# Performance work log

Measured on AMD Instinct MI355X. Metric: run time of the kernel, lower is better.

The kernel has to match this reference:

```python
import jax, jax.numpy as jnp
import numpy as np

E = 512      # embed dim
H = 8        # heads
DH = E // H  # dim per head
LN_EPS = 1e-5


def _sinusoidal_pe(pos_seq, embed_dim):
    # pos_seq: (L,) float; returns (L, embed_dim)
    inv_freq = 1.0 / (10000.0 ** (jnp.arange(0.0, embed_dim, 2.0, dtype=jnp.float32) / embed_dim))
    sin_inp = jnp.outer(pos_seq, inv_freq)                     # (L, Dh/2)
    return jnp.concatenate([jnp.sin(sin_inp), jnp.cos(sin_inp)], axis=-1)


def _rel_shift_bhij(x, k_len):
    # x: (B, H, T, L) -> left-shift trick -> (B, H, T, k_len)
    b, h, t, l = x.shape
    x = jnp.pad(x, ((0, 0), (0, 0), (0, 0), (1, 0)))           # (B,H,T,L+1)
    x = x.reshape(b, h, l + 1, t)
    x = x[:, :, 1:, :]
    x = x.reshape(b, h, t, l)
    return x[:, :, :, :k_len]


def setup_inputs() -> dict:
    key = jax.random.key(0)
    ks = jax.random.split(key, 10)
    B, T = 8, 1024
    xav = np.sqrt(6.0 / (E + E))  # xavier_uniform bound for (E,E)
    return {
        "input_tensor": jax.random.normal(ks[0], (B, T, E), jnp.float32),
        "sequence_mask": jnp.ones((B, T), dtype=bool),
        "ln_scale": jnp.ones((E,), jnp.float32),
        "ln_bias": jnp.zeros((E,), jnp.float32),
        "q_w": jax.random.uniform(ks[1], (E, E), jnp.float32, -xav, xav),
        "k_w": jax.random.uniform(ks[2], (E, E), jnp.float32, -xav, xav),
        "v_w": jax.random.uniform(ks[3], (E, E), jnp.float32, -xav, xav),
        "in_proj_bias": jax.random.normal(ks[4], (3 * E,), jnp.float32) * 0.02,
        "out_w": jax.random.uniform(ks[5], (E, E), jnp.float32, -xav, xav),
        "out_b": jnp.zeros((E,), jnp.float32),
        "pos_bias_u": jax.random.normal(ks[6], (H, DH), jnp.float32) * 0.02,
        "pos_bias_v": jax.random.normal(ks[7], (H, DH), jnp.float32) * 0.02,
    }


def reference(input_tensor, sequence_mask, ln_scale, ln_bias, q_w, k_w, v_w,
              in_proj_bias, out_w, out_b, pos_bias_u, pos_bias_v):
    B, T, _ = input_tensor.shape
    # LayerNorm
    mu = jnp.mean(input_tensor, axis=-1, keepdims=True)
    var = jnp.mean(jnp.square(input_tensor - mu), axis=-1, keepdims=True)
    x = (input_tensor - mu) * jax.lax.rsqrt(var + LN_EPS) * ln_scale + ln_bias

    # note: torch code unpacks in_proj_bias as (bias_k, bias_q, bias_v)
    bias_k, bias_q, bias_v = jnp.split(in_proj_bias, 3)
    q = (x @ q_w.T + bias_q).reshape(B, T, H, DH)
    k = (x @ k_w.T + bias_k).reshape(B, T, H, DH)
    v = (x @ v_w.T + bias_v).reshape(B, T, H, DH)

    # sinusoidal relative PE: positions T-1 .. -(T-1), shape (2T-1, Dh)
    pos_seq = jnp.arange(T - 1, -T, -1, dtype=jnp.float32)
    rel_pe = _sinusoidal_pe(pos_seq, DH)

    q_u = q + pos_bias_u  # (B,T,H,Dh)
    q_v = q + pos_bias_v

    attn_ac = jnp.einsum('bihf,bjhf->bhij', q_u, k)            # (B,H,T,T)
    attn_bd = jnp.einsum('bihf,jf->bhij', q_v, rel_pe)         # (B,H,T,2T-1)
    attn_bd = _rel_shift_bhij(attn_bd, k_len=T)                # (B,H,T,T)

    mask = jnp.where(sequence_mask[:, None, None, :], 0.0, -jnp.inf).astype(input_tensor.dtype)
    attn = (attn_ac + attn_bd + mask) * (1.0 / np.sqrt(DH))
    weights = jax.nn.softmax(attn, axis=-1)

    out = jnp.einsum('bhij,bjhf->bihf', weights, v).reshape(B, T, E)
    return out @ out_w.T + out_b
```

## Files before the change

kernel.cpp:

```cpp
#include <hip/hip_runtime.h>
#include <hip/hip_bf16.h>
#include <cstdint>
#include <cstddef>


typedef __attribute__((ext_vector_type(8))) short bf16x8;
typedef __attribute__((ext_vector_type(4))) float f32x4;
typedef __attribute__((ext_vector_type(4))) unsigned short usht4;

#define MFMA(a, b, c) __builtin_amdgcn_mfma_f32_16x16x32_bf16((a), (b), (c), 0, 0, 0)

__device__ __forceinline__ unsigned short f2bf(float f) {
    __bf16 h = (__bf16)f;
    union { __bf16 h; unsigned short u; } v; v.h = h;
    return v.u;
}

__device__ __forceinline__ float exp2r(float x) {
    float r; asm("v_exp_f32 %0, %1" : "=v"(r) : "v"(x)); return r;
}

__device__ __forceinline__ void gload16(void* lds, const void* g) {
    __builtin_amdgcn_global_load_lds((const __attribute__((address_space(1))) void*)g,
                                     (__attribute__((address_space(3))) void*)lds,
                                     16, 0, 0);
}

__global__ __launch_bounds__(256) void prep_ln_kernel(const float* __restrict__ qw,
                                                      const float* __restrict__ kw,
                                                      const float* __restrict__ vw,
                                                      const float* __restrict__ ow,
                                                      const float* __restrict__ x,
                                                      const float* __restrict__ gam,
                                                      const float* __restrict__ bet,
                                                      unsigned short* __restrict__ wcat,
                                                      unsigned short* __restrict__ kptab,
                                                      float* __restrict__ qsc,
                                                      unsigned short* __restrict__ xout) {
    const int bid = blockIdx.x;
    if (bid < 4096) {
        const int which = bid >> 10;
        const int idx = (bid & 1023) * 256 + threadIdx.x;
        const float* src = (which == 0) ? qw : (which == 1) ? kw : (which == 2) ? vw : ow;
        wcat[which * 262144 + idx] = f2bf(src[idx]);
        return;
    }
    if (bid < 4352) {
        const int idx = (bid - 4096) * 256 + threadIdx.x;
        const int t = idx >> 6, f6 = idx & 63, f = f6 & 31;
        const float w = powf(10000.0f, -(float)f * (1.0f / 32.0f));
        const float ang = (float)t * w;
        const float sv = sinf(ang), cv = cosf(ang);
        qsc[t * 64 + 2 * f + ((f6 < 32) ? 0 : 1)] = (f6 < 32) ? sv : cv;
        kptab[idx] = f2bf((f6 < 32) ? cv : sv);
        return;
    }
    const int row = (bid - 4352) * 4 + (threadIdx.x >> 6);
    const int lane = threadIdx.x & 63;
    const float4* xr = (const float4*)(x + (size_t)row * 512);
    float4 a = xr[lane];
    float4 b = xr[lane + 64];
    float s  = a.x + a.y + a.z + a.w + b.x + b.y + b.z + b.w;
    float ss = a.x*a.x + a.y*a.y + a.z*a.z + a.w*a.w
             + b.x*b.x + b.y*b.y + b.z*b.z + b.w*b.w;
#pragma unroll
    for (int m = 1; m < 64; m <<= 1) {
        s  += __shfl_xor(s, m);
        ss += __shfl_xor(ss, m);
    }
    const float mu   = s * (1.0f / 512.0f);
    const float rstd = rsqrtf(ss * (1.0f / 512.0f) - mu * mu + 1e-5f);
    const float4* g4 = (const float4*)gam;
    const float4* b4 = (const float4*)bet;
    float4 g0 = g4[lane], g1 = g4[lane + 64];
    float4 c0 = b4[lane], c1 = b4[lane + 64];
    usht4 o0, o1;
    o0[0] = f2bf((a.x - mu) * rstd * g0.x + c0.x);
    o0[1] = f2bf((a.y - mu) * rstd * g0.y + c0.y);
    o0[2] = f2bf((a.z - mu) * rstd * g0.z + c0.z);
    o0[3] = f2bf((a.w - mu) * rstd * g0.w + c0.w);
    o1[0] = f2bf((b.x - mu) * rstd * g1.x + c1.x);
    o1[1] = f2bf((b.y - mu) * rstd * g1.y + c1.y);
    o1[2] = f2bf((b.z - mu) * rstd * g1.z + c1.z);
    o1[3] = f2bf((b.w - mu) * rstd * g1.w + c1.w);
    *(usht4*)&xout[(size_t)row * 512 + lane * 4] = o0;
    *(usht4*)&xout[(size_t)row * 512 + 256 + lane * 4] = o1;
}

#define GEMM_PROLOGUE()                                                        \
    __shared__ __align__(16) unsigned short As[2][128 * 64];                   \
    __shared__ __align__(16) unsigned short Bs[2][128 * 64];                   \
    const int tid = threadIdx.x;                                               \
    const int wid = tid >> 6;                                                  \
    const int lane = tid & 63;                                                 \
    const int wr = wid >> 1, wc = wid & 1;                                     \
    const int c = lane & 15, hi = lane >> 4;                                   \
    f32x4 acc[4][4];                                                           \
    _Pragma("unroll") for (int i = 0; i < 4; ++i)                              \
        _Pragma("unroll") for (int j = 0; j < 4; ++j) acc[i][j] = 0.0f;        \
    const int rbase = wid * 8;                                                 \
    const int sl = lane & 7;                                                   \
    const int lrow = lane >> 3;                                                \
    auto stageAB = [&](int buf, int kt) {                                      \
        const int k0 = kt * 64;                                                \
        _Pragma("unroll") for (int ch = 0; ch < 4; ++ch) {                     \
            const int rr = ch * 32 + rbase + lrow;                             \
            const int soff = (sl * 8) ^ ((rr & 7) << 3);                       \
            gload16(&As[buf][(ch * 32 + rbase) * 64],                          \
                    A + (size_t)(m0 + rr) * 512 + k0 + soff);                  \
            gload16(&Bs[buf][(ch * 32 + rbase) * 64],                          \
                    Bw + (size_t)(n0 + rr) * 512 + k0 + soff);                 \
        }                                                                      \
    };                                                                         \
    stageAB(0, 0);                                                             \
    __syncthreads();                                                           \
    int cb = 0;                                                                \
    for (int kt = 0; kt < 8; ++kt) {                                           \
        if (kt < 7) stageAB(cb ^ 1, kt + 1);                                   \
        _Pragma("unroll") for (int ks = 0; ks < 2; ++ks) {                     \
            bf16x8 af[4], bfr[4];                                              \
            _Pragma("unroll") for (int mf = 0; mf < 4; ++mf) {                 \
                const int ar = wr * 64 + mf * 16 + c;                          \
                const int ko = (ks * 32 + hi * 8) ^ ((ar & 7) << 3);           \
                af[mf] = *(const bf16x8*)&As[cb][ar * 64 + ko];                \
            }                                                                  \
            _Pragma("unroll") for (int nf = 0; nf < 4; ++nf) {                 \
                const int br = wc * 64 + nf * 16 + c;                          \
                const int ko = (ks * 32 + hi * 8) ^ ((br & 7) << 3);           \
                bfr[nf] = *(const bf16x8*)&Bs[cb][br * 64 + ko];               \
            }                                                                  \
            _Pragma("unroll") for (int mf = 0; mf < 4; ++mf)                   \
                _Pragma("unroll") for (int nf = 0; nf < 4; ++nf)               \
                    acc[mf][nf] = MFMA(af[mf], bfr[nf], acc[mf][nf]);          \
        }                                                                      \
        __syncthreads();                                                       \
        cb ^= 1;                                                               \
    }                                                                          \
    const int mb = m0 + wr * 64;                                               \
    const int nb = n0 + wc * 64;

__global__ __launch_bounds__(256) void gemm_qkv_kernel(const unsigned short* __restrict__ A,
                                                       const unsigned short* __restrict__ Bw,
                                                       const float* __restrict__ ipb,
                                                       const float* __restrict__ pbu,
                                                       const float* __restrict__ pbv,
                                                       const float* __restrict__ qsc,
                                                       unsigned short* __restrict__ qu,
                                                       unsigned short* __restrict__ qp,
                                                       unsigned short* __restrict__ kk,
                                                       unsigned short* __restrict__ vT) {
    const int m0 = blockIdx.x * 128;
    const int n0 = blockIdx.y * 128;
    const int nsec = blockIdx.y >> 2;
    GEMM_PROLOGUE()

    const float SCALE = 0.125f * 1.44269504088896340736f;

    if (nsec == 0) {
#pragma unroll
        for (int mf = 0; mf < 4; ++mf) {
#pragma unroll
            for (int r = 0; r < 4; ++r) {
                const int gm = mb + mf * 16 + hi * 4 + r;
                const int t = gm & 1023;
#pragma unroll
                for (int p = 0; p < 2; ++p) {
                    const int fl = p * 16 + c;
                    const int gn1 = nb + fl;
                    const int gn2 = gn1 + 32;
                    const float v1 = acc[mf][p][r]     + ipb[512 + gn1];
                    const float v2 = acc[mf][p + 2][r] + ipb[512 + gn2];
                    qu[(size_t)gm * 512 + gn1] = f2bf((v1 + pbu[gn1]) * SCALE);
                    qu[(size_t)gm * 512 + gn2] = f2bf((v2 + pbu[gn2]) * SCALE);
                    const float qvs = v1 + pbv[gn1];
                    const float qvc = v2 + pbv[gn2];
                    const float2 sc2 = *(const float2*)&qsc[t * 64 + 2 * fl];
                    qp[(size_t)gm * 512 + gn1] = f2bf((qvs * sc2.x + qvc * sc2.y) * SCALE);
                    qp[(size_t)gm * 512 + gn2] = f2bf((qvc * sc2.x - qvs * sc2.y) * SCALE);
                }
            }
        }
    } else if (nsec == 1) {
#pragma unroll
        for (int mf = 0; mf < 4; ++mf)
#pragma unroll
            for (int nf = 0; nf < 4; ++nf) {
                const int gm = mb + mf * 16 + hi * 4;
                const int gn = nb + nf * 16 + c;
                const float bia = ipb[gn - 512];
#pragma unroll
                for (int r = 0; r < 4; ++r)
                    kk[(size_t)(gm + r) * 512 + (gn - 512)] = f2bf(acc[mf][nf][r] + bia);
            }
    } else {
#pragma unroll
        for (int mf = 0; mf < 4; ++mf)
#pragma unroll
            for (int nf = 0; nf < 4; ++nf) {
                const int gm = mb + mf * 16 + hi * 4;
                const int gn = nb + nf * 16 + c;
                const float bia = ipb[gn];
                const int bb = gm >> 10;
                const int t  = gm & 1023;
                usht4 pk;
#pragma unroll
                for (int r = 0; r < 4; ++r) pk[r] = f2bf(acc[mf][nf][r] + bia);
                *(usht4*)&vT[((size_t)bb * 512 + (gn - 1024)) * 1024 + t] = pk;
            }
    }
}

__global__ __launch_bounds__(256) void gemm_out_kernel(const unsigned short* __restrict__ A,
                                                       const unsigned short* __restrict__ Bw,
                                                       const float* __restrict__ bias,
                                                       float* __restrict__ outf) {
    const int m0 = blockIdx.x * 128;
    const int n0 = blockIdx.y * 128;
    GEMM_PROLOGUE()
#pragma unroll
    for (int mf = 0; mf < 4; ++mf)
#pragma unroll
        for (int nf = 0; nf < 4; ++nf) {
            const int gm = mb + mf * 16 + hi * 4;
            const int gn = nb + nf * 16 + c;
            const float bia = bias[gn];
#pragma unroll
            for (int r = 0; r < 4; ++r)
                outf[(size_t)(gm + r) * 512 + gn] = acc[mf][nf][r] + bia;
        }
}

__global__ __launch_bounds__(512, 4) void attn_kernel(const unsigned short* __restrict__ qu,
                                                      const unsigned short* __restrict__ qp,
                                                      const unsigned short* __restrict__ kk,
                                                      const unsigned short* __restrict__ vT,
                                                      const unsigned short* __restrict__ kptab,
                                                      unsigned short* __restrict__ att) {
    __shared__ __align__(16) char smem[67584];
    char* kbuf = smem;
    char* pbuf = smem + 16384;
    char* vbuf = smem + 32768;
    unsigned short* pw = (unsigned short*)(smem + 49152) + (threadIdx.x >> 6) * (16 * 72);

    const int tid = threadIdx.x;
    const int w = tid >> 6, lane = tid & 63;
    const int c = lane & 15, hi = lane >> 4;
    const int id = blockIdx.x;
    const int b = id & 7, h = (id >> 3) & 7, it = id >> 6;
    const int iw = it * 128 + w * 16;

    const size_t qbase = ((size_t)b * 1024 + iw) * 512 + h * 64;
    bf16x8 quf[4];
#pragma unroll
    for (int ks = 0; ks < 2; ++ks) {
        const size_t o = qbase + (size_t)c * 512 + ks * 32 + hi * 8;
        quf[ks]     = *(const bf16x8*)&qu[o];
        quf[ks + 2] = *(const bf16x8*)&qp[o];
    }

    f32x4 oacc[4];
    float mrun[4], lrun[4];
#pragma unroll
    for (int nf = 0; nf < 4; ++nf) oacc[nf] = 0.0f;
#pragma unroll
    for (int r = 0; r < 4; ++r) { mrun[r] = -1e30f; lrun[r] = 0.0f; }

    bf16x8 ones;
#pragma unroll
    for (int i = 0; i < 8; ++i) ones[i] = (short)0x3F80;

    int off2[2][4];
#pragma unroll
    for (int nf = 0; nf < 4; ++nf) {
        const int r = nf * 16 + c;
        const int sw = (r & 7) << 4;
        off2[0][nf] = r * 128 + ((hi * 16) ^ sw);
        off2[1][nf] = r * 128 + ((64 + hi * 16) ^ sw);
    }

    const size_t kbase = ((size_t)b * 1024) * 512 + h * 64;
    const size_t vbase = ((size_t)b * 512 + h * 64) * 1024;

    const int srow = tid >> 3;
    const int scol = ((tid & 7) * 16) ^ ((srow & 7) << 4);
    const char* ksrc = (const char*)(kk + kbase + (size_t)srow * 512) + scol;
    const char* psrc = (const char*)(kptab + (size_t)srow * 64) + scol;
    const char* vsrc = (const char*)(vT + vbase + (size_t)srow * 1024) + scol;

    auto stage = [&](int buf, int jt) {
        gload16(kbuf + buf * 8192 + w * 1024, ksrc + (size_t)jt * 65536);
        gload16(pbuf + buf * 8192 + w * 1024, psrc + (size_t)jt * 8192);
        gload16(vbuf + buf * 8192 + w * 1024, vsrc + (size_t)jt * 128);
    };

    stage(0, 0);
    __syncthreads();
    int cur = 0;

    for (int jt = 0; jt < 16; ++jt) {
        if (jt < 15) stage(cur ^ 1, jt + 1);

        const char* kb = kbuf + cur * 8192;
        const char* pb = pbuf + cur * 8192;
        const char* vb = vbuf + cur * 8192;

        f32x4 s[4];
#pragma unroll
        for (int nf = 0; nf < 4; ++nf) s[nf] = 0.0f;
#pragma unroll
        for (int ks = 0; ks < 4; ++ks) {
            const char* base = (ks < 2) ? kb : pb;
            bf16x8 kfr[4];
#pragma unroll
            for (int nf = 0; nf < 4; ++nf)
                kfr[nf] = *(const bf16x8*)(base + off2[ks & 1][nf]);
#pragma unroll
            for (int nf = 0; nf < 4; ++nf)
                s[nf] = MFMA(quf[ks], kfr[nf], s[nf]);
        }

        float lm[4];
        bool allok = true;
#pragma unroll
        for (int r = 0; r < 4; ++r) {
            lm[r] = fmaxf(fmaxf(s[0][r], s[1][r]), fmaxf(s[2][r], s[3][r]));
            allok = allok && (lm[r] <= mrun[r] + 8.0f);
        }
        if (!__all(allok)) {
#pragma unroll
            for (int r = 0; r < 4; ++r) {
                float pm = lm[r];
                pm = fmaxf(pm, __shfl_xor(pm, 1));
                pm = fmaxf(pm, __shfl_xor(pm, 2));
                pm = fmaxf(pm, __shfl_xor(pm, 4));
                pm = fmaxf(pm, __shfl_xor(pm, 8));
                const float mn = fmaxf(mrun[r], pm);
                const float sc = exp2r(mrun[r] - mn);
                mrun[r] = mn;
                lrun[r] *= sc;
#pragma unroll
                for (int nf = 0; nf < 4; ++nf) oacc[nf][r] *= sc;
            }
        }

#pragma unroll
        for (int nf = 0; nf < 4; ++nf)
#pragma unroll
            for (int r = 0; r < 4; ++r)
                pw[(hi * 4 + r) * 72 + nf * 16 + c] = f2bf(exp2r(s[nf][r] - mrun[r]));

        f32x4 psum = 0.0f;
#pragma unroll
        for (int ks = 0; ks < 2; ++ks) {
            const bf16x8 pa = *(const bf16x8*)&pw[c * 72 + ks * 32 + hi * 8];
            bf16x8 vfr[4];
#pragma unroll
            for (int nf = 0; nf < 4; ++nf)
                vfr[nf] = *(const bf16x8*)(vb + off2[ks][nf]);
#pragma unroll
            for (int nf = 0; nf < 4; ++nf)
                oacc[nf] = MFMA(pa, vfr[nf], oacc[nf]);
            psum = MFMA(pa, ones, psum);
        }
#pragma unroll
        for (int r = 0; r < 4; ++r) lrun[r] += psum[r];

        __syncthreads();
        cur ^= 1;
    }

#pragma unroll
    for (int r = 0; r < 4; ++r) {
        const float inv = 1.0f / lrun[r];
#pragma unroll
        for (int nf = 0; nf < 4; ++nf)
            att[((size_t)b * 1024 + iw + hi * 4 + r) * 512 + h * 64 + nf * 16 + c] =
                f2bf(oacc[nf][r] * inv);
    }
}

extern "C" void kernel_launch(void* const* d_in, const int* in_sizes, int n_in,
                              void* d_out, int out_size, void* d_ws, size_t ws_size,
                              hipStream_t stream) {
    const float* x_in = (const float*)d_in[0];
    const float* ln_g = (const float*)d_in[2];
    const float* ln_b = (const float*)d_in[3];
    const float* q_w  = (const float*)d_in[4];
    const float* k_w  = (const float*)d_in[5];
    const float* v_w  = (const float*)d_in[6];
    const float* ipb  = (const float*)d_in[7];
    const float* o_w  = (const float*)d_in[8];
    const float* o_b  = (const float*)d_in[9];
    const float* pbu  = (const float*)d_in[10];
    const float* pbv  = (const float*)d_in[11];
    float* out = (float*)d_out;

    char* ws = (char*)d_ws;
    unsigned short* xb    = (unsigned short*)(ws);
    unsigned short* qu    = (unsigned short*)(ws + 8388608);
    unsigned short* qp    = (unsigned short*)(ws + 16777216);
    unsigned short* kk    = (unsigned short*)(ws + 25165824);
    unsigned short* vT    = (unsigned short*)(ws + 33554432);
    unsigned short* wcat  = (unsigned short*)(ws + 41943040);
    unsigned short* kptab = (unsigned short*)(ws + 44040192);
    float*          qsc   = (float*)(ws + 44171264);
    unsigned short* att   = xb;

    prep_ln_kernel<<<dim3(6400), 256, 0, stream>>>(q_w, k_w, v_w, o_w, x_in, ln_g, ln_b,
                                                   wcat, kptab, qsc, xb);
    gemm_qkv_kernel<<<dim3(64, 12), 256, 0, stream>>>(xb, wcat, ipb, pbu, pbv, qsc,
                                                      qu, qp, kk, vT);
    attn_kernel<<<dim3(512), 512, 0, stream>>>(qu, qp, kk, vT, kptab, att);
    gemm_out_kernel<<<dim3(64, 4), 256, 0, stream>>>(att, wcat + 786432, o_b, out);
}
```

Baseline: 86.03 us.

## Give each attention wave two 16-row query tiles, halving block threads

The attention kernel now launches 256-thread blocks in which each wave processes 32 query rows as two 16-row MFMA tiles instead of one. Each K/positional/V fragment read from LDS is reused across both tiles, and each thread issues two staging loads per buffer so the block still fills the same 128-row tile. This cuts LDS fragment reads per MFMA and the number of waves synchronising at each barrier. In exchange it doubles the accumulator and softmax-state registers per thread, which may lower occupancy and latency hiding.

```diff
diff --git a/kernel.cpp b/kernel.cpp
--- a/kernel.cpp
+++ b/kernel.cpp
@@ -230,7 +230,7 @@
         }
 }
 
-__global__ __launch_bounds__(512, 4) void attn_kernel(const unsigned short* __restrict__ qu,
+__global__ __launch_bounds__(256, 2) void attn_kernel(const unsigned short* __restrict__ qu,
                                                       const unsigned short* __restrict__ qp,
                                                       const unsigned short* __restrict__ kk,
                                                       const unsigned short* __restrict__ vT,
@@ -240,30 +240,35 @@
     char* kbuf = smem;
     char* pbuf = smem + 16384;
     char* vbuf = smem + 32768;
-    unsigned short* pw = (unsigned short*)(smem + 49152) + (threadIdx.x >> 6) * (16 * 72);
+    unsigned short* pw = (unsigned short*)(smem + 49152) + (threadIdx.x >> 6) * (32 * 72);
 
     const int tid = threadIdx.x;
     const int w = tid >> 6, lane = tid & 63;
     const int c = lane & 15, hi = lane >> 4;
     const int id = blockIdx.x;
     const int b = id & 7, h = (id >> 3) & 7, it = id >> 6;
-    const int iw = it * 128 + w * 16;
+    const int iw = it * 128 + w * 32;
 
     const size_t qbase = ((size_t)b * 1024 + iw) * 512 + h * 64;
-    bf16x8 quf[4];
-#pragma unroll
-    for (int ks = 0; ks < 2; ++ks) {
-        const size_t o = qbase + (size_t)c * 512 + ks * 32 + hi * 8;
-        quf[ks]     = *(const bf16x8*)&qu[o];
-        quf[ks + 2] = *(const bf16x8*)&qp[o];
-    }
-
-    f32x4 oacc[4];
-    float mrun[4], lrun[4];
-#pragma unroll
-    for (int nf = 0; nf < 4; ++nf) oacc[nf] = 0.0f;
-#pragma unroll
-    for (int r = 0; r < 4; ++r) { mrun[r] = -1e30f; lrun[r] = 0.0f; }
+    bf16x8 quf[2][4];
+#pragma unroll
+    for (int mi = 0; mi < 2; ++mi)
+#pragma unroll
+        for (int ks = 0; ks < 2; ++ks) {
+            const size_t o = qbase + (size_t)(mi * 16 + c) * 512 + ks * 32 + hi * 8;
+            quf[mi][ks]     = *(const bf16x8*)&qu[o];
+            quf[mi][ks + 2] = *(const bf16x8*)&qp[o];
+        }
+
+    f32x4 oacc[2][4];
+    float mrun[2][4], lrun[2][4];
+#pragma unroll
+    for (int mi = 0; mi < 2; ++mi) {
+#pragma unroll
+        for (int nf = 0; nf < 4; ++nf) oacc[mi][nf] = 0.0f;
+#pragma unroll
+        for (int r = 0; r < 4; ++r) { mrun[mi][r] = -1e30f; lrun[mi][r] = 0.0f; }
+    }
 
     bf16x8 ones;
 #pragma unroll
@@ -283,14 +288,23 @@
 
     const int srow = tid >> 3;
     const int scol = ((tid & 7) * 16) ^ ((srow & 7) << 4);
-    const char* ksrc = (const char*)(kk + kbase + (size_t)srow * 512) + scol;
-    const char* psrc = (const char*)(kptab + (size_t)srow * 64) + scol;
-    const char* vsrc = (const char*)(vT + vbase + (size_t)srow * 1024) + scol;
+    const char* ksrc  = (const char*)(kk + kbase + (size_t)srow * 512) + scol;
+    const char* ksrc2 = ksrc + 32 * 1024;
+    const char* psrc  = (const char*)(kptab + (size_t)srow * 64) + scol;
+    const char* psrc2 = psrc + 32 * 128;
+    const char* vsrc  = (const char*)(vT + vbase + (size_t)srow * 1024) + scol;
+    const char* vsrc2 = vsrc + 32 * 2048;
 
     auto stage = [&](int buf, int jt) {
-        gload16(kbuf + buf * 8192 + w * 1024, ksrc + (size_t)jt * 65536);
-        gload16(pbuf + buf * 8192 + w * 1024, psrc + (size_t)jt * 8192);
-        gload16(vbuf + buf * 8192 + w * 1024, vsrc + (size_t)jt * 128);
+        const size_t ko = (size_t)jt * 65536;
+        const size_t po = (size_t)jt * 8192;
+        const size_t vo = (size_t)jt * 128;
+        gload16(kbuf + buf * 8192 + w * 1024,        ksrc  + ko);
+        gload16(kbuf + buf * 8192 + 4096 + w * 1024, ksrc2 + ko);
+        gload16(pbuf + buf * 8192 + w * 1024,        psrc  + po);
+        gload16(pbuf + buf * 8192 + 4096 + w * 1024, psrc2 + po);
+        gload16(vbuf + buf * 8192 + w * 1024,        vsrc  + vo);
+        gload16(vbuf + buf * 8192 + 4096 + w * 1024, vsrc2 + vo);
     };
 
     stage(0, 0);
@@ -304,9 +318,11 @@
         const char* pb = pbuf + cur * 8192;
         const char* vb = vbuf + cur * 8192;
 
-        f32x4 s[4];
-#pragma unroll
-        for (int nf = 0; nf < 4; ++nf) s[nf] = 0.0f;
+        f32x4 s[2][4];
+#pragma unroll
+        for (int mi = 0; mi < 2; ++mi)
+#pragma unroll
+            for (int nf = 0; nf < 4; ++nf) s[mi][nf] = 0.0f;
 #pragma unroll
         for (int ks = 0; ks < 4; ++ks) {
             const char* base = (ks < 2) ? kb : pb;
@@ -315,68 +331,88 @@
             for (int nf = 0; nf < 4; ++nf)
                 kfr[nf] = *(const bf16x8*)(base + off2[ks & 1][nf]);
 #pragma unroll
+            for (int mi = 0; mi < 2; ++mi)
+#pragma unroll
+                for (int nf = 0; nf < 4; ++nf)
+                    s[mi][nf] = MFMA(quf[mi][ks], kfr[nf], s[mi][nf]);
+        }
+
+        bool allok = true;
+        float lm[2][4];
+#pragma unroll
+        for (int mi = 0; mi < 2; ++mi)
+#pragma unroll
+            for (int r = 0; r < 4; ++r) {
+                lm[mi][r] = fmaxf(fmaxf(s[mi][0][r], s[mi][1][r]),
+                                  fmaxf(s[mi][2][r], s[mi][3][r]));
+                allok = allok && (lm[mi][r] <= mrun[mi][r] + 8.0f);
+            }
+        if (!__all(allok)) {
+#pragma unroll
+            for (int mi = 0; mi < 2; ++mi)
+#pragma unroll
+                for (int r = 0; r < 4; ++r) {
+                    float pm = lm[mi][r];
+                    pm = fmaxf(pm, __shfl_xor(pm, 1));
+                    pm = fmaxf(pm, __shfl_xor(pm, 2));
+                    pm = fmaxf(pm, __shfl_xor(pm, 4));
+                    pm = fmaxf(pm, __shfl_xor(pm, 8));
+                    const float mn = fmaxf(mrun[mi][r], pm);
+                    const float sc = exp2r(mrun[mi][r] - mn);
+                    mrun[mi][r] = mn;
+                    lrun[mi][r] *= sc;
+#pragma unroll
+                    for (int nf = 0; nf < 4; ++nf) oacc[mi][nf][r] *= sc;
+                }
+        }
+
+#pragma unroll
+        for (int mi = 0; mi < 2; ++mi)
+#pragma unroll
             for (int nf = 0; nf < 4; ++nf)
-                s[nf] = MFMA(quf[ks], kfr[nf], s[nf]);
-        }
-
-        float lm[4];
-        bool allok = true;
-#pragma unroll
-        for (int r = 0; r < 4; ++r) {
-            lm[r] = fmaxf(fmaxf(s[0][r], s[1][r]), fmaxf(s[2][r], s[3][r]));
-            allok = allok && (lm[r] <= mrun[r] + 8.0f);
-        }
-        if (!__all(allok)) {
-#pragma unroll
-            for (int r = 0; r < 4; ++r) {
-                float pm = lm[r];
-                pm = fmaxf(pm, __shfl_xor(pm, 1));
-                pm = fmaxf(pm, __shfl_xor(pm, 2));
-                pm = fmaxf(pm, __shfl_xor(pm, 4));
-                pm = fmaxf(pm, __shfl_xor(pm, 8));
-                const float mn = fmaxf(mrun[r], pm);
-                const float sc = exp2r(mrun[r] - mn);
-                mrun[r] = mn;
-                lrun[r] *= sc;
-#pragma unroll
-                for (int nf = 0; nf < 4; ++nf) oacc[nf][r] *= sc;
-            }
-        }
-
-#pragma unroll
-        for (int nf = 0; nf < 4; ++nf)
-#pragma unroll
-            for (int r = 0; r < 4; ++r)
-                pw[(hi * 4 + r) * 72 + nf * 16 + c] = f2bf(exp2r(s[nf][r] - mrun[r]));
-
-        f32x4 psum = 0.0f;
+#pragma unroll
+                for (int r = 0; r < 4; ++r)
+                    pw[(mi * 16 + hi * 4 + r) * 72 + nf * 16 + c] =
+                        f2bf(exp2r(s[mi][nf][r] - mrun[mi][r]));
+
+        f32x4 psum[2] = {0.0f, 0.0f};
 #pragma unroll
         for (int ks = 0; ks < 2; ++ks) {
-            const bf16x8 pa = *(const bf16x8*)&pw[c * 72 + ks * 32 + hi * 8];
+            bf16x8 pa[2];
+#pragma unroll
+            for (int mi = 0; mi < 2; ++mi)
+                pa[mi] = *(const bf16x8*)&pw[(mi * 16 + c) * 72 + ks * 32 + hi * 8];
             bf16x8 vfr[4];
 #pragma unroll
             for (int nf = 0; nf < 4; ++nf)
                 vfr[nf] = *(const bf16x8*)(vb + off2[ks][nf]);
 #pragma unroll
-            for (int nf = 0; nf < 4; ++nf)
-                oacc[nf] = MFMA(pa, vfr[nf], oacc[nf]);
-            psum = MFMA(pa, ones, psum);
-        }
-#pragma unroll
-        for (int r = 0; r < 4; ++r) lrun[r] += psum[r];
+            for (int mi = 0; mi < 2; ++mi) {
+#pragma unroll
+                for (int nf = 0; nf < 4; ++nf)
+                    oacc[mi][nf] = MFMA(pa[mi], vfr[nf], oacc[mi][nf]);
+                psum[mi] = MFMA(pa[mi], ones, psum[mi]);
+            }
+        }
+#pragma unroll
+        for (int mi = 0; mi < 2; ++mi)
+#pragma unroll
+            for (int r = 0; r < 4; ++r) lrun[mi][r] += psum[mi][r];
 
         __syncthreads();
         cur ^= 1;
     }
 
 #pragma unroll
-    for (int r = 0; r < 4; ++r) {
-        const float inv = 1.0f / lrun[r];
-#pragma unroll
-        for (int nf = 0; nf < 4; ++nf)
-            att[((size_t)b * 1024 + iw + hi * 4 + r) * 512 + h * 64 + nf * 16 + c] =
-                f2bf(oacc[nf][r] * inv);
-    }
+    for (int mi = 0; mi < 2; ++mi)
+#pragma unroll
+        for (int r = 0; r < 4; ++r) {
+            const float inv = 1.0f / lrun[mi][r];
+#pragma unroll
+            for (int nf = 0; nf < 4; ++nf)
+                att[((size_t)b * 1024 + iw + mi * 16 + hi * 4 + r) * 512 + h * 64 + nf * 16 + c] =
+                    f2bf(oacc[mi][nf][r] * inv);
+        }
 }
 
 extern "C" void kernel_launch(void* const* d_in, const int* in_sizes, int n_in,
@@ -410,6 +446,6 @@
                                                    wcat, kptab, qsc, xb);
     gemm_qkv_kernel<<<dim3(64, 12), 256, 0, stream>>>(xb, wcat, ipb, pbu, pbv, qsc,
                                                       qu, qp, kk, vT);
-    attn_kernel<<<dim3(512), 512, 0, stream>>>(qu, qp, kk, vT, kptab, att);
+    attn_kernel<<<dim3(512), 256, 0, stream>>>(qu, qp, kk, vT, kptab, att);
     gemm_out_kernel<<<dim3(64, 4), 256, 0, stream>>>(att, wcat + 786432, o_b, out);
 }
```

After: 88.00 us. +2.3%, slower.
